# Performance work log

Hardware: AMD Instinct MI355X
Metric: run time of the kernel (lower is better)

Reference implementation:

```python
import jax, jax.numpy as jnp
import numpy as np

NUM_QUBITS = 13
NUM_LAYERS = 2


def setup_inputs() -> dict:
    key = jax.random.key(0)
    k1, k2 = jax.random.split(key)
    x = jax.random.normal(k1, (512, 2 ** NUM_QUBITS), dtype=jnp.float32)
    weights = jax.random.normal(k2, (NUM_LAYERS, NUM_QUBITS, 3), dtype=jnp.float32)
    return {"x": x, "weights": weights}


def _rot_matrix(phi, theta, omega):
    # qml.Rot(phi, theta, omega) = RZ(omega) @ RY(theta) @ RZ(phi)
    c = jnp.cos(theta * 0.5).astype(jnp.complex64)
    s = jnp.sin(theta * 0.5).astype(jnp.complex64)
    e_m = jnp.exp((-0.5j) * (phi + omega).astype(jnp.complex64))
    e_p = jnp.exp((0.5j) * (phi + omega).astype(jnp.complex64))
    e_d = jnp.exp((0.5j) * (phi - omega).astype(jnp.complex64))
    e_dc = jnp.exp((-0.5j) * (phi - omega).astype(jnp.complex64))
    row0 = jnp.stack([e_m * c, -e_d * s])
    row1 = jnp.stack([e_dc * s, e_p * c])
    return jnp.stack([row0, row1])  # (2, 2) complex64


def _apply_1q(psi, U, q):
    # psi: (B, 2, 2, ..., 2); contract qubit axis q with 2x2 gate U
    ax = 1 + q
    psi = jnp.moveaxis(psi, ax, -1)
    psi = psi @ U.T
    return jnp.moveaxis(psi, -1, ax)


def _apply_cnot(psi, c, t):
    # X on target where control bit == 1
    s0 = jax.lax.index_in_dim(psi, 0, axis=1 + c, keepdims=True)
    s1 = jax.lax.index_in_dim(psi, 1, axis=1 + c, keepdims=True)
    s1 = jnp.flip(s1, axis=1 + t)
    return jnp.concatenate([s0, s1], axis=1 + c)


def reference(x, weights):
    n = NUM_QUBITS
    B = x.shape[0]
    # AmplitudeEmbedding with normalize=True
    norm = jnp.sqrt(jnp.sum(x * x, axis=1, keepdims=True))
    psi = (x / norm).astype(jnp.complex64).reshape((B,) + (2,) * n)
    # StronglyEntanglingLayers (default ranges r_l = (l % (n-1)) + 1, CNOT imprimitive)
    for l in range(NUM_LAYERS):
        r = (l % (n - 1)) + 1
        for q in range(n):
            U = _rot_matrix(weights[l, q, 0], weights[l, q, 1], weights[l, q, 2])
            psi = _apply_1q(psi, U, q)
        for q in range(n):
            psi = _apply_cnot(psi, q, (q + r) % n)
    # expval(PauliZ(n // 2)) = p(bit=0) - p(bit=1)
    m = n // 2
    probs = jnp.real(psi) ** 2 + jnp.imag(psi) ** 2
    axes = tuple(i for i in range(1, n + 1) if i != 1 + m)
    p = probs.sum(axis=axes)  # (B, 2)
    return p[:, 0] - p[:, 1]
```

## Files before the change

### kernel.cpp

```cpp
#include <hip/hip_runtime.h>
#include <math.h>

#define NQ    13
#define DIM   8192
#define BLOCK 512
#define NGATE 26

__device__ __forceinline__ int SW(int a) { return a ^ (((a >> 7) & 7) << 2); }

struct PCols { int c[NQ]; };
constexpr PCols make_cols(int r) {
    PCols P{};
    for (int b = 0; b < NQ; ++b) {
        int cc = 1 << b;
        for (int cq = 0; cq < NQ; ++cq) {
            const int cb = 12 - cq;
            const int tb = 12 - ((cq + r) % NQ);
            cc ^= ((cc >> cb) & 1) << tb;
        }
        P.c[b] = cc;
    }
    return P;
}
constexpr PCols C1 = make_cols(1);
constexpr int make_rm6() {
    int m = 0;
    for (int b = 0; b < NQ; ++b) m |= ((make_cols(2).c[b] >> 6) & 1) << b;
    return m;
}
constexpr int RM6 = make_rm6();

struct Combos { int k[16]; };
constexpr Combos make_combos() {
    Combos K{};
    for (int j = 0; j < 16; ++j)
        K.k[j] = ((j & 1) ? C1.c[0] : 0) ^ ((j & 2) ? C1.c[1] : 0)
               ^ ((j & 4) ? C1.c[10] : 0) ^ ((j & 8) ? C1.c[11] : 0);
    return K;
}
constexpr Combos KC = make_combos();

constexpr int make_sjw() {
    int wv = 0;
    for (int j = 0; j < 16; ++j) {
        const int jm = (j & 3) | (((j >> 2) & 3) << 10);
        wv |= (__builtin_popcount(jm & RM6) & 1) << j;
    }
    return wv;
}
constexpr int SJW = make_sjw();

__device__ __forceinline__ float2 f2mul(float s, float2 a) {
    return make_float2(s * a.x, s * a.y);
}
__device__ __forceinline__ float2 f2fma(float s, float2 a, float2 b) {
    return make_float2(fmaf(s, a.x, b.x), fmaf(s, a.y, b.y));
}
__device__ __forceinline__ float2 fswap(float2 a) { return make_float2(-a.y, a.x); }

template<int P>
__device__ __forceinline__ void rotp(float2* c, const float* __restrict__ g) {
    const float ur00 = g[0], ui00 = g[1], ur01 = g[2], ui01 = g[3];
    const float ur10 = g[4], ui10 = g[5], ur11 = g[6], ui11 = g[7];
    #pragma unroll
    for (int m = 0; m < 8; ++m) {
        const int j0 = ((m >> P) << (P + 1)) | (m & ((1 << P) - 1));
        const int j1 = j0 | (1 << P);
        const float2 a0 = c[j0], a1 = c[j1];
        const float2 s0 = fswap(a0), s1 = fswap(a1);
        c[j0] = f2fma(ui01, s1, f2fma(ur01, a1, f2fma(ui00, s0, f2mul(ur00, a0))));
        c[j1] = f2fma(ui11, s1, f2fma(ur11, a1, f2fma(ui10, s0, f2mul(ur10, a0))));
    }
}

template<int CTRL>
__device__ __forceinline__ float dppx(float v) {
    return __int_as_float(
        __builtin_amdgcn_update_dpp(0, __float_as_int(v), CTRL, 0xf, 0xf, true));
}
template<int CTRL>
__device__ __forceinline__ void rotlane(float2* c, const float* __restrict__ g, const bool hi) {
    const float Ar = hi ? g[6] : g[0];
    const float Ai = hi ? g[7] : g[1];
    const float Br = hi ? g[4] : g[2];
    const float Bi = hi ? g[5] : g[3];
    #pragma unroll
    for (int j = 0; j < 16; ++j) {
        const float2 p  = make_float2(dppx<CTRL>(c[j].x), dppx<CTRL>(c[j].y));
        const float2 so = fswap(c[j]), sp = fswap(p);
        c[j] = f2fma(Bi, sp, f2fma(Br, p, f2fma(Ai, so, f2mul(Ar, c[j]))));
    }
}

__device__ __forceinline__ void loadgrp(const float* re, const float* im, int a, float2* c) {
    const float4 r = *(const float4*)&re[a];
    const float4 i = *(const float4*)&im[a];
    c[0] = make_float2(r.x, i.x); c[1] = make_float2(r.y, i.y);
    c[2] = make_float2(r.z, i.z); c[3] = make_float2(r.w, i.w);
}
__device__ __forceinline__ void storegrp(float* re, float* im, int a, const float2* c) {
    *(float4*)&re[a] = make_float4(c[0].x, c[1].x, c[2].x, c[3].x);
    *(float4*)&im[a] = make_float4(c[0].y, c[1].y, c[2].y, c[3].y);
}

__global__ __launch_bounds__(BLOCK, 4) void qsim_kernel(
    const float* __restrict__ x,
    const float* __restrict__ w,
    float* __restrict__ out)
{
    __shared__ __align__(16) float re[DIM];
    __shared__ __align__(16) float im[DIM];
    __shared__ float gm[NGATE * 8];
    __shared__ float red[BLOCK / 64];

    const int b = blockIdx.x;
    const int t = threadIdx.x;

    if (t < NGATE) {
        const float phi = w[t * 3 + 0], theta = w[t * 3 + 1], omega = w[t * 3 + 2];
        float co, si;  sincosf(0.5f * theta, &si, &co);
        float sps, cps, sds, cds;
        sincosf(0.5f * (phi + omega), &sps, &cps);
        sincosf(0.5f * (phi - omega), &sds, &cds);
        float* g = &gm[t * 8];
        g[0] =  cps * co;  g[1] = -sps * co;
        g[2] = -cds * si;  g[3] = -sds * si;
        g[4] =  cds * si;  g[5] = -sds * si;
        g[6] =  cps * co;  g[7] =  sps * co;
    }

    const float4* x4 = (const float4*)(x + (size_t)b * DIM);
    float ss = 0.f;
    #pragma unroll
    for (int k = 0; k < 4; ++k) {
        const int m = t + BLOCK * k;
        const int a = SW(4 * m);
        const float4 v = x4[m];
        *(float4*)&re[a] = v;
        *(float4*)&im[a] = make_float4(0.f, 0.f, 0.f, 0.f);
        ss += v.x * v.x + v.y * v.y + v.z * v.z + v.w * v.w;
    }
    #pragma unroll
    for (int off = 32; off > 0; off >>= 1) ss += __shfl_down(ss, off, 64);
    if ((t & 63) == 0) red[t >> 6] = ss;
    __syncthreads();
    float total = 0.f;
    #pragma unroll
    for (int i = 0; i < BLOCK / 64; ++i) total += red[i];

    float2 c[16];

    const int base2 = (((t >> 2) & 15) << 2) | ((t & 3) << 8) | (((t >> 6) & 7) << 10);
    const int base3 = (((t >> 1) & 255) << 2) | ((t & 1) << 12);

    #pragma unroll
    for (int l = 0; l < 2; ++l) {
        const float* G = gm + l * 13 * 8;

        #pragma unroll
        for (int g = 0; g < 4; ++g) loadgrp(re, im, SW((t << 4) | (g << 2)), &c[4 * g]);
        rotp<0>(c, G + 12 * 8);
        rotp<1>(c, G + 11 * 8);
        rotp<2>(c, G + 10 * 8);
        rotp<3>(c, G +  9 * 8);
        rotlane<0xB1>(c, G + 8 * 8, (t & 1) != 0);
        rotlane<0x4E>(c, G + 7 * 8, (t & 2) != 0);
        #pragma unroll
        for (int g = 0; g < 4; ++g) storegrp(re, im, SW((t << 4) | (g << 2)), &c[4 * g]);
        __syncthreads();

        #pragma unroll
        for (int h = 0; h < 4; ++h) loadgrp(re, im, SW(base2 | (h << 6)), &c[4 * h]);
        rotp<2>(c, G + 6 * 8);
        rotp<3>(c, G + 5 * 8);
        rotlane<0xB1>(c, G + 4 * 8, (t & 1) != 0);
        rotlane<0x4E>(c, G + 3 * 8, (t & 2) != 0);
        #pragma unroll
        for (int h = 0; h < 4; ++h) storegrp(re, im, SW(base2 | (h << 6)), &c[4 * h]);
        __syncthreads();

        #pragma unroll
        for (int h = 0; h < 4; ++h) loadgrp(re, im, SW(base3 | (h << 10)), &c[4 * h]);
        __syncthreads();
        rotp<2>(c, G + 2 * 8);
        rotp<3>(c, G + 1 * 8);
        rotlane<0xB1>(c, G + 0 * 8, (t & 1) != 0);

        if (l == 0) {
            int mb = 0;
            if (t & 1) mb ^= C1.c[12];
            #pragma unroll
            for (int bb = 0; bb < 8; ++bb)
                if ((t >> (bb + 1)) & 1) mb ^= C1.c[2 + bb];
            #pragma unroll
            for (int j = 0; j < 16; ++j) {
                const int a = SW(mb ^ KC.k[j]);
                re[a] = c[j].x; im[a] = c[j].y;
            }
            __syncthreads();
        }
    }

    const int sbase = __popc(base3 & RM6) & 1;
    float acc = 0.f;
    #pragma unroll
    for (int j = 0; j < 16; ++j) {
        const float p = c[j].x * c[j].x + c[j].y * c[j].y;
        acc += (sbase ^ ((SJW >> j) & 1)) ? -p : p;
    }
    #pragma unroll
    for (int off = 32; off > 0; off >>= 1) acc += __shfl_down(acc, off, 64);
    if ((t & 63) == 0) red[t >> 6] = acc;
    __syncthreads();
    if (t == 0) {
        float tot = 0.f;
        #pragma unroll
        for (int i = 0; i < BLOCK / 64; ++i) tot += red[i];
        out[b] = tot / total;
    }
}

extern "C" void kernel_launch(void* const* d_in, const int* in_sizes, int n_in,
                              void* d_out, int out_size, void* d_ws, size_t ws_size,
                              hipStream_t stream) {
    const float* x = (const float*)d_in[0];
    const float* w = (const float*)d_in[1];
    float* out = (float*)d_out;
    const int B = in_sizes[0] / DIM;
    qsim_kernel<<<B, BLOCK, 0, stream>>>(x, w, out);
}
```

Before: 85.40 us.

## Restructure qubit passes: interleaved complex LDS, load input directly to registers, fewer passes

Stores the state vector as interleaved complex pairs in one LDS array and reads the input straight into registers, which removes the initial LDS write of re/im. Uses cross-row DPP mirror/reverse combinations so that four lane-level qubits are handled per pass. Each layer therefore needs two LDS passes instead of three, and the gate coefficients are fetched as float4 pairs and applied with packed v2f arithmetic. The price is more complex DPP permutations and new index bookkeeping that has to be correct.

```diff
diff --git a/kernel.cpp b/kernel.cpp
--- a/kernel.cpp
+++ b/kernel.cpp
@@ -5,6 +5,8 @@
 #define DIM   8192
 #define BLOCK 512
 #define NGATE 26
+
+typedef float v2f __attribute__((ext_vector_type(2)));
 
 __device__ __forceinline__ int SW(int a) { return a ^ (((a >> 7) & 7) << 2); }
 
@@ -22,7 +24,7 @@
     }
     return P;
 }
-constexpr PCols C1 = make_cols(1);
+constexpr PCols C1c = make_cols(1);
 constexpr int make_rm6() {
     int m = 0;
     for (int b = 0; b < NQ; ++b) m |= ((make_cols(2).c[b] >> 6) & 1) << b;
@@ -34,8 +36,8 @@
 constexpr Combos make_combos() {
     Combos K{};
     for (int j = 0; j < 16; ++j)
-        K.k[j] = ((j & 1) ? C1.c[0] : 0) ^ ((j & 2) ? C1.c[1] : 0)
-               ^ ((j & 4) ? C1.c[10] : 0) ^ ((j & 8) ? C1.c[11] : 0);
+        K.k[j] = ((j & 1) ? C1c.c[0] : 0) ^ ((j & 2) ? C1c.c[8] : 0)
+               ^ ((j & 4) ? C1c.c[9] : 0) ^ ((j & 8) ? C1c.c[10] : 0);
     return K;
 }
 constexpr Combos KC = make_combos();
@@ -43,64 +45,92 @@
 constexpr int make_sjw() {
     int wv = 0;
     for (int j = 0; j < 16; ++j) {
-        const int jm = (j & 3) | (((j >> 2) & 3) << 10);
+        const int jm = (j & 1) | (((j >> 1) & 7) << 8);
         wv |= (__builtin_popcount(jm & RM6) & 1) << j;
     }
     return wv;
 }
 constexpr int SJW = make_sjw();
 
-__device__ __forceinline__ float2 f2mul(float s, float2 a) {
-    return make_float2(s * a.x, s * a.y);
-}
-__device__ __forceinline__ float2 f2fma(float s, float2 a, float2 b) {
-    return make_float2(fmaf(s, a.x, b.x), fmaf(s, a.y, b.y));
-}
-__device__ __forceinline__ float2 fswap(float2 a) { return make_float2(-a.y, a.x); }
+struct GPair { float4 a, b; };
+__device__ __forceinline__ GPair ldg8(const float* gm, int gi) {
+    GPair g;
+    g.a = *(const float4*)&gm[gi * 8];
+    g.b = *(const float4*)&gm[gi * 8 + 4];
+    return g;
+}
 
 template<int P>
-__device__ __forceinline__ void rotp(float2* c, const float* __restrict__ g) {
-    const float ur00 = g[0], ui00 = g[1], ur01 = g[2], ui01 = g[3];
-    const float ur10 = g[4], ui10 = g[5], ur11 = g[6], ui11 = g[7];
+__device__ __forceinline__ void rotp(v2f* c, const GPair g) {
     #pragma unroll
     for (int m = 0; m < 8; ++m) {
         const int j0 = ((m >> P) << (P + 1)) | (m & ((1 << P) - 1));
         const int j1 = j0 | (1 << P);
-        const float2 a0 = c[j0], a1 = c[j1];
-        const float2 s0 = fswap(a0), s1 = fswap(a1);
-        c[j0] = f2fma(ui01, s1, f2fma(ur01, a1, f2fma(ui00, s0, f2mul(ur00, a0))));
-        c[j1] = f2fma(ui11, s1, f2fma(ur11, a1, f2fma(ui10, s0, f2mul(ur10, a0))));
-    }
-}
+        const v2f a0 = c[j0], a1 = c[j1];
+        const v2f s0 = { -a0.y, a0.x };
+        const v2f s1 = { -a1.y, a1.x };
+        c[j0] = g.a.x * a0 + g.a.y * s0 + g.a.z * a1 + g.a.w * s1;
+        c[j1] = g.b.x * a0 + g.b.y * s0 + g.b.z * a1 + g.b.w * s1;
+    }
+}
+
+#define DPP_XOR1 0xB1
+#define DPP_XOR2 0x4E
+#define DPP_QREV 0x1B
+#define DPP_HMIR 0x141
+#define DPP_MIR  0x140
 
 template<int CTRL>
-__device__ __forceinline__ float dppx(float v) {
+__device__ __forceinline__ float dpp1(float v) {
     return __int_as_float(
         __builtin_amdgcn_update_dpp(0, __float_as_int(v), CTRL, 0xf, 0xf, true));
 }
-template<int CTRL>
-__device__ __forceinline__ void rotlane(float2* c, const float* __restrict__ g, const bool hi) {
-    const float Ar = hi ? g[6] : g[0];
-    const float Ai = hi ? g[7] : g[1];
-    const float Br = hi ? g[4] : g[2];
-    const float Bi = hi ? g[5] : g[3];
+template<int CA, int CB>
+__device__ __forceinline__ float dppx(float v) {
+    float r = dpp1<CA>(v);
+    if constexpr (CB >= 0) r = dpp1<CB>(r);
+    return r;
+}
+
+template<int CA, int CB>
+__device__ __forceinline__ void rotlane(v2f* c, const GPair g, const bool hi) {
+    const float Ar = hi ? g.b.z : g.a.x;
+    const float Ai = hi ? g.b.w : g.a.y;
+    const float Br = hi ? g.b.x : g.a.z;
+    const float Bi = hi ? g.b.y : g.a.w;
     #pragma unroll
     for (int j = 0; j < 16; ++j) {
-        const float2 p  = make_float2(dppx<CTRL>(c[j].x), dppx<CTRL>(c[j].y));
-        const float2 so = fswap(c[j]), sp = fswap(p);
-        c[j] = f2fma(Bi, sp, f2fma(Br, p, f2fma(Ai, so, f2mul(Ar, c[j]))));
-    }
-}
-
-__device__ __forceinline__ void loadgrp(const float* re, const float* im, int a, float2* c) {
-    const float4 r = *(const float4*)&re[a];
-    const float4 i = *(const float4*)&im[a];
-    c[0] = make_float2(r.x, i.x); c[1] = make_float2(r.y, i.y);
-    c[2] = make_float2(r.z, i.z); c[3] = make_float2(r.w, i.w);
-}
-__device__ __forceinline__ void storegrp(float* re, float* im, int a, const float2* c) {
-    *(float4*)&re[a] = make_float4(c[0].x, c[1].x, c[2].x, c[3].x);
-    *(float4*)&im[a] = make_float4(c[0].y, c[1].y, c[2].y, c[3].y);
+        v2f p;
+        p.x = dppx<CA, CB>(c[j].x);
+        p.y = dppx<CA, CB>(c[j].y);
+        const v2f so = { -c[j].y, c[j].x };
+        const v2f sp = { -p.y, p.x };
+        c[j] = Ar * c[j] + Ai * so + Br * p + Bi * sp;
+    }
+}
+
+__device__ __forceinline__ void p1_load(const float* st, int t, v2f* c) {
+    #pragma unroll
+    for (int g = 0; g < 8; ++g) {
+        const float4 v = *(const float4*)&st[SW((t << 5) | (g << 2))];
+        c[2 * g]     = { v.x, v.y };
+        c[2 * g + 1] = { v.z, v.w };
+    }
+}
+__device__ __forceinline__ void p1_store(float* st, int t, const v2f* c) {
+    #pragma unroll
+    for (int g = 0; g < 8; ++g) {
+        const float4 v = { c[2 * g].x, c[2 * g].y, c[2 * g + 1].x, c[2 * g + 1].y };
+        *(float4*)&st[SW((t << 5) | (g << 2))] = v;
+    }
+}
+__device__ __forceinline__ void p2_load(const float* st, int base, v2f* c) {
+    #pragma unroll
+    for (int g = 0; g < 8; ++g) {
+        const float4 v = *(const float4*)&st[SW(base | (g << 9))];
+        c[2 * g]     = { v.x, v.y };
+        c[2 * g + 1] = { v.z, v.w };
+    }
 }
 
 __global__ __launch_bounds__(BLOCK, 4) void qsim_kernel(
@@ -108,10 +138,9 @@
     const float* __restrict__ w,
     float* __restrict__ out)
 {
-    __shared__ __align__(16) float re[DIM];
-    __shared__ __align__(16) float im[DIM];
-    __shared__ float gm[NGATE * 8];
-    __shared__ float red[BLOCK / 64];
+    __shared__ __align__(16) float st[2 * DIM];
+    __shared__ __align__(16) float gm[NGATE * 8];
+    __shared__ float red_ss[8], red_acc[8];
 
     const int b = blockIdx.x;
     const int t = threadIdx.x;
@@ -130,78 +159,79 @@
     }
 
     const float4* x4 = (const float4*)(x + (size_t)b * DIM);
+    v2f c[16];
     float ss = 0.f;
     #pragma unroll
     for (int k = 0; k < 4; ++k) {
-        const int m = t + BLOCK * k;
-        const int a = SW(4 * m);
-        const float4 v = x4[m];
-        *(float4*)&re[a] = v;
-        *(float4*)&im[a] = make_float4(0.f, 0.f, 0.f, 0.f);
+        const float4 v = x4[(t << 2) | k];
+        c[4 * k + 0] = { v.x, 0.f };
+        c[4 * k + 1] = { v.y, 0.f };
+        c[4 * k + 2] = { v.z, 0.f };
+        c[4 * k + 3] = { v.w, 0.f };
         ss += v.x * v.x + v.y * v.y + v.z * v.z + v.w * v.w;
     }
     #pragma unroll
     for (int off = 32; off > 0; off >>= 1) ss += __shfl_down(ss, off, 64);
-    if ((t & 63) == 0) red[t >> 6] = ss;
-    __syncthreads();
-    float total = 0.f;
-    #pragma unroll
-    for (int i = 0; i < BLOCK / 64; ++i) total += red[i];
-
-    float2 c[16];
-
-    const int base2 = (((t >> 2) & 15) << 2) | ((t & 3) << 8) | (((t >> 6) & 7) << 10);
-    const int base3 = (((t >> 1) & 255) << 2) | ((t & 1) << 12);
-
-    #pragma unroll
-    for (int l = 0; l < 2; ++l) {
-        const float* G = gm + l * 13 * 8;
-
+    if ((t & 63) == 0) red_ss[t >> 6] = ss;
+    __syncthreads();
+
+    const int p2base = (((t >> 2) & 127) << 2) | ((t & 3) << 12);
+
+    rotp<0>(c, ldg8(gm, 12));
+    rotp<1>(c, ldg8(gm, 11));
+    rotp<2>(c, ldg8(gm, 10));
+    rotp<3>(c, ldg8(gm,  9));
+    rotlane<DPP_XOR1, -1>(c, ldg8(gm, 8), (t & 1) != 0);
+    rotlane<DPP_XOR2, -1>(c, ldg8(gm, 7), (t & 2) != 0);
+    rotlane<DPP_HMIR, DPP_QREV>(c, ldg8(gm, 6), (t & 4) != 0);
+    rotlane<DPP_MIR,  DPP_HMIR>(c, ldg8(gm, 5), (t & 8) != 0);
+    p1_store(st, t, c);
+    __syncthreads();
+
+    p2_load(st, p2base, c);
+    rotp<1>(c, ldg8(gm, 4));
+    rotp<2>(c, ldg8(gm, 3));
+    rotp<3>(c, ldg8(gm, 2));
+    rotlane<DPP_XOR1, -1>(c, ldg8(gm, 1), (t & 1) != 0);
+    rotlane<DPP_XOR2, -1>(c, ldg8(gm, 0), (t & 2) != 0);
+    __syncthreads();
+
+    {
+        int mb = 0;
         #pragma unroll
-        for (int g = 0; g < 4; ++g) loadgrp(re, im, SW((t << 4) | (g << 2)), &c[4 * g]);
-        rotp<0>(c, G + 12 * 8);
-        rotp<1>(c, G + 11 * 8);
-        rotp<2>(c, G + 10 * 8);
-        rotp<3>(c, G +  9 * 8);
-        rotlane<0xB1>(c, G + 8 * 8, (t & 1) != 0);
-        rotlane<0x4E>(c, G + 7 * 8, (t & 2) != 0);
+        for (int k = 0; k < 7; ++k)
+            if ((t >> (2 + k)) & 1) mb ^= C1c.c[1 + k];
+        if (t & 1) mb ^= C1c.c[11];
+        if (t & 2) mb ^= C1c.c[12];
         #pragma unroll
-        for (int g = 0; g < 4; ++g) storegrp(re, im, SW((t << 4) | (g << 2)), &c[4 * g]);
-        __syncthreads();
-
-        #pragma unroll
-        for (int h = 0; h < 4; ++h) loadgrp(re, im, SW(base2 | (h << 6)), &c[4 * h]);
-        rotp<2>(c, G + 6 * 8);
-        rotp<3>(c, G + 5 * 8);
-        rotlane<0xB1>(c, G + 4 * 8, (t & 1) != 0);
-        rotlane<0x4E>(c, G + 3 * 8, (t & 2) != 0);
-        #pragma unroll
-        for (int h = 0; h < 4; ++h) storegrp(re, im, SW(base2 | (h << 6)), &c[4 * h]);
-        __syncthreads();
-
-        #pragma unroll
-        for (int h = 0; h < 4; ++h) loadgrp(re, im, SW(base3 | (h << 10)), &c[4 * h]);
-        __syncthreads();
-        rotp<2>(c, G + 2 * 8);
-        rotp<3>(c, G + 1 * 8);
-        rotlane<0xB1>(c, G + 0 * 8, (t & 1) != 0);
-
-        if (l == 0) {
-            int mb = 0;
-            if (t & 1) mb ^= C1.c[12];
-            #pragma unroll
-            for (int bb = 0; bb < 8; ++bb)
-                if ((t >> (bb + 1)) & 1) mb ^= C1.c[2 + bb];
-            #pragma unroll
-            for (int j = 0; j < 16; ++j) {
-                const int a = SW(mb ^ KC.k[j]);
-                re[a] = c[j].x; im[a] = c[j].y;
-            }
-            __syncthreads();
+        for (int j = 0; j < 16; ++j) {
+            const int a = SW(2 * (mb ^ KC.k[j]));
+            *(v2f*)&st[a] = c[j];
         }
     }
-
-    const int sbase = __popc(base3 & RM6) & 1;
+    __syncthreads();
+
+    p1_load(st, t, c);
+    rotp<0>(c, ldg8(gm, 13 + 12));
+    rotp<1>(c, ldg8(gm, 13 + 11));
+    rotp<2>(c, ldg8(gm, 13 + 10));
+    rotp<3>(c, ldg8(gm, 13 +  9));
+    rotlane<DPP_XOR1, -1>(c, ldg8(gm, 13 + 8), (t & 1) != 0);
+    rotlane<DPP_XOR2, -1>(c, ldg8(gm, 13 + 7), (t & 2) != 0);
+    rotlane<DPP_HMIR, DPP_QREV>(c, ldg8(gm, 13 + 6), (t & 4) != 0);
+    rotlane<DPP_MIR,  DPP_HMIR>(c, ldg8(gm, 13 + 5), (t & 8) != 0);
+    p1_store(st, t, c);
+    __syncthreads();
+
+    p2_load(st, p2base, c);
+    rotp<1>(c, ldg8(gm, 13 + 4));
+    rotp<2>(c, ldg8(gm, 13 + 3));
+    rotp<3>(c, ldg8(gm, 13 + 2));
+    rotlane<DPP_XOR1, -1>(c, ldg8(gm, 13 + 1), (t & 1) != 0);
+    rotlane<DPP_XOR2, -1>(c, ldg8(gm, 13 + 0), (t & 2) != 0);
+
+    const int fixed = ((((t >> 2) & 127) << 1) | ((t & 3) << 11));
+    const int sbase = __popc(fixed & RM6) & 1;
     float acc = 0.f;
     #pragma unroll
     for (int j = 0; j < 16; ++j) {
@@ -210,13 +240,13 @@
     }
     #pragma unroll
     for (int off = 32; off > 0; off >>= 1) acc += __shfl_down(acc, off, 64);
-    if ((t & 63) == 0) red[t >> 6] = acc;
+    if ((t & 63) == 0) red_acc[t >> 6] = acc;
     __syncthreads();
     if (t == 0) {
-        float tot = 0.f;
+        float ta = 0.f, ts = 0.f;
         #pragma unroll
-        for (int i = 0; i < BLOCK / 64; ++i) tot += red[i];
-        out[b] = tot / total;
+        for (int i = 0; i < 8; ++i) { ta += red_acc[i]; ts += red_ss[i]; }
+        out[b] = ta / ts;
     }
 }
 
```

Result: slower. 93.26 us (+9.2%).
